# Optimization experiments

Measured on AMD Instinct MI355X. Metric: run time of the kernel, lower is better.

The kernel has to match this reference:

```python
import jax, jax.numpy as jnp
import numpy as np
import math

B, S, D = 4, 2048, 512
H, DK, DV = 8, 12, 32

def setup_inputs() -> dict:
    key = jax.random.key(0)
    ks = jax.random.split(key, 12)
    s = 0.02
    return {
        "query": jax.random.normal(ks[0], (B, S, D), jnp.float32),
        "key": jax.random.normal(ks[1], (B, S, D), jnp.float32),
        "value": jax.random.normal(ks[2], (B, S, D), jnp.float32),
        "mask": jax.random.randint(ks[3], (B, 1, S), 0, 2, jnp.int32),
        "Wq": jax.random.normal(ks[4], (D, H * DK), jnp.float32) * s,
        "bq": jnp.zeros((H * DK,), jnp.float32),
        "Wk": jax.random.normal(ks[5], (D, H * DK), jnp.float32) * s,
        "bk": jnp.zeros((H * DK,), jnp.float32),
        "Wv": jax.random.normal(ks[6], (D, H * DV), jnp.float32) * s,
        "bv": jnp.zeros((H * DV,), jnp.float32),
        "Wx": jax.random.normal(ks[7], (H * DV, D), jnp.float32) * s,
        "bx": jnp.zeros((D,), jnp.float32),
    }

def reference(query, key, value, mask, Wq, bq, Wk, bk, Wv, bv, Wx, bx):
    # mask: (B,1,S) -> (B,1,1,S) after unsqueeze(1)
    m = mask[:, None, :, :]  # (B,1,1,S)
    nb = query.shape[0]
    # projections, split heads: (B, S, H*dk) -> (B, H, S, dk)
    q = (query @ Wq + bq).reshape(nb, -1, H, DK).transpose(0, 2, 1, 3)
    k = (key @ Wk + bk).reshape(nb, -1, H, DK).transpose(0, 2, 1, 3)
    v = (value @ Wv + bv).reshape(nb, -1, H, DV).transpose(0, 2, 1, 3)
    scores = jnp.einsum("bhqd,bhkd->bhqk", q, k) / math.sqrt(DK)
    scores = jnp.where(m == 0, jnp.float32(-1e9), scores)
    p_attn = jax.nn.softmax(scores, axis=-1)
    # dropout is identity in eval mode
    x = jnp.einsum("bhqk,bhkd->bhqd", p_attn, v)  # (B,H,S,dv)
    x = x.transpose(0, 2, 1, 3).reshape(nb, -1, H * DV)
    x = x @ Wx + bx
    return (x, p_attn)
```

## Files before the change

kernel.cpp:

```cpp
#include <hip/hip_runtime.h>
#include <math.h>

#define S_LEN 2048
#define NB 4
#define NH 8

typedef short bfrag8 __attribute__((ext_vector_type(8)));
typedef float f32x16 __attribute__((ext_vector_type(16)));
typedef float f32x4 __attribute__((ext_vector_type(4)));

#if __has_builtin(__builtin_amdgcn_exp2f)
#define EXP2(x) __builtin_amdgcn_exp2f(x)
#else
#define EXP2(x) exp2f(x)
#endif

__device__ __forceinline__ unsigned short f2bf(float x) {
  union { float f; unsigned u; } v; v.f = x;
  unsigned r = v.u + 0x7FFFu + ((v.u >> 16) & 1u);
  return (unsigned short)(r >> 16);
}

__global__ __launch_bounds__(256) void transpose_w(
    const float* __restrict__ Wq, const float* __restrict__ Wk,
    const float* __restrict__ Wv, const float* __restrict__ Wx,
    unsigned short* __restrict__ wqT, unsigned short* __restrict__ wkT,
    unsigned short* __restrict__ wvT, unsigned short* __restrict__ wxT)
{
  int i = blockIdx.x * 256 + threadIdx.x;
  if (i < 49152) {
    const int n = i / 512, kk = i % 512;
    wqT[i] = f2bf(Wq[(size_t)kk * 96 + n]);
  } else if (i < 98304) {
    i -= 49152; const int n = i / 512, kk = i % 512;
    wkT[i] = f2bf(Wk[(size_t)kk * 96 + n]);
  } else if (i < 229376) {
    i -= 98304; const int n = i / 512, kk = i % 512;
    wvT[i] = f2bf(Wv[(size_t)kk * 256 + n]);
  } else if (i < 360448) {
    i -= 229376; const int n = i / 256, kk = i % 256;
    wxT[i] = f2bf(Wx[(size_t)kk * 512 + n]);
  }
}

__global__ __launch_bounds__(256) void proj_qkv(
    const float* __restrict__ query, const float* __restrict__ key_,
    const float* __restrict__ value, const int* __restrict__ mask,
    const unsigned short* __restrict__ wqT, const unsigned short* __restrict__ wkT,
    const unsigned short* __restrict__ wvT,
    const float* __restrict__ bq, const float* __restrict__ bk,
    const float* __restrict__ bv,
    unsigned short* __restrict__ q_bf, unsigned short* __restrict__ k_bf,
    unsigned short* __restrict__ vT_bf, float qscale)
{
  const int id = blockIdx.x;
  const int xcd = id & 7, j = id >> 3;
  const int bxl = j & 7, ys = j >> 3;
  const int bx = xcd * 8 + bxl;
  const int t = threadIdx.x, w = t >> 6, lane = t & 63;
  const int lo = lane & 31, hi = lane >> 5;
  const int r0 = bx * 128 + 32 * w;

  if (ys < 6) {
    const bool isq = (ys < 3);
    const float* A = isq ? query : key_;
    const unsigned short* BT = isq ? wqT : wkT;
    const float* bias = isq ? bq : bk;
    unsigned short* Cb = isq ? q_bf : k_bf;
    const float osc = isq ? qscale : 1.0f;
    const int c0 = (isq ? ys : ys - 3) * 32;

    const float* ap = A + (size_t)(r0 + lo) * 512 + hi * 8;
    const unsigned short* bp = BT + (size_t)(c0 + lo) * 512 + hi * 8;

    f32x16 acc;
#pragma unroll
    for (int r = 0; r < 16; ++r) acc[r] = 0.f;

    for (int k0 = 0; k0 < 512; k0 += 16) {
      const float4 a0 = *reinterpret_cast<const float4*>(ap + k0);
      const float4 a1 = *reinterpret_cast<const float4*>(ap + k0 + 4);
      bfrag8 af;
      af[0] = (short)f2bf(a0.x); af[1] = (short)f2bf(a0.y);
      af[2] = (short)f2bf(a0.z); af[3] = (short)f2bf(a0.w);
      af[4] = (short)f2bf(a1.x); af[5] = (short)f2bf(a1.y);
      af[6] = (short)f2bf(a1.z); af[7] = (short)f2bf(a1.w);
      const bfrag8 bf = *reinterpret_cast<const bfrag8*>(bp + k0);
      acc = __builtin_amdgcn_mfma_f32_32x32x16_bf16(af, bf, acc, 0, 0, 0);
    }

    const int c = c0 + lo;
    const int off = (c / 12) * 16 + (c % 12);
    const float bc = bias[c];
#pragma unroll
    for (int r = 0; r < 16; ++r) {
      const int grow = r0 + (r & 3) + 8 * (r >> 2) + 4 * hi;
      Cb[(size_t)grow * 128 + off] = f2bf((acc[r] + bc) * osc);
    }
    if ((c % 12) == 0) {
      const int hh = c / 12;
#pragma unroll
      for (int r = 0; r < 16; ++r) {
        const int grow = r0 + (r & 3) + 8 * (r >> 2) + 4 * hi;
        ushort4 pv;
        pv.x = isq ? (unsigned short)0x3F80
                   : ((mask[grow] != 0) ? (unsigned short)0
                                        : (unsigned short)0xCE6E);
        pv.y = 0; pv.z = 0; pv.w = 0;
        *reinterpret_cast<ushort4*>(Cb + (size_t)grow * 128 + hh * 16 + 12) = pv;
      }
    }
  } else {
    const int ct0 = (ys - 6) * 128;
    const float* ap = value + (size_t)(r0 + lo) * 512 + hi * 8;
    const unsigned short* bp = wvT + (size_t)(ct0 + lo) * 512 + hi * 8;

    f32x16 acc[4];
#pragma unroll
    for (int tt = 0; tt < 4; ++tt)
#pragma unroll
      for (int r = 0; r < 16; ++r) acc[tt][r] = 0.f;

    for (int k0 = 0; k0 < 512; k0 += 16) {
      const float4 a0 = *reinterpret_cast<const float4*>(ap + k0);
      const float4 a1 = *reinterpret_cast<const float4*>(ap + k0 + 4);
      bfrag8 af;
      af[0] = (short)f2bf(a0.x); af[1] = (short)f2bf(a0.y);
      af[2] = (short)f2bf(a0.z); af[3] = (short)f2bf(a0.w);
      af[4] = (short)f2bf(a1.x); af[5] = (short)f2bf(a1.y);
      af[6] = (short)f2bf(a1.z); af[7] = (short)f2bf(a1.w);
#pragma unroll
      for (int tt = 0; tt < 4; ++tt) {
        const bfrag8 bf = *reinterpret_cast<const bfrag8*>(
            bp + (size_t)tt * 32 * 512 + k0);
        acc[tt] = __builtin_amdgcn_mfma_f32_32x32x16_bf16(bf, af, acc[tt], 0, 0, 0);
      }
    }

    const int s = r0 + lo;
    const int bb = s >> 11, sl = s & (S_LEN - 1);
#pragma unroll
    for (int tt = 0; tt < 4; ++tt) {
#pragma unroll
      for (int r = 0; r < 16; ++r) {
        const int c = ct0 + tt * 32 + (r & 3) + 8 * (r >> 2) + 4 * hi;
        vT_bf[((size_t)(bb * 256 + c)) * S_LEN + sl] = f2bf(acc[tt][r] + bv[c]);
      }
    }
  }
}

__global__ __launch_bounds__(256) void attn_mfma(
    const unsigned short* __restrict__ q_bf,
    const unsigned short* __restrict__ k_bf,
    const unsigned short* __restrict__ vT_bf,
    float* __restrict__ p_out, unsigned short* __restrict__ x_bf)
{
  const int id = blockIdx.x + blockIdx.y * 64;
  const int xcd = id & 7, jj = id >> 3;
  const int bh = 4 * xcd + (jj >> 6);
  const int q0 = (jj & 63) * 32;
  const int b = bh >> 3, h = bh & 7;
  const int t = threadIdx.x, w = t >> 6, lane = t & 63;
  const int lo = lane & 31, hi = lane >> 5;

  __shared__ float red_lds[4][32];
  __shared__ __align__(16) char smbuf[4 * 32 * 68 * 4];
  float (*p_lds)[32][68] = reinterpret_cast<float (*)[32][68]>(smbuf);
  float (*xr)[64][20]    = reinterpret_cast<float (*)[64][20]>(smbuf);

  const bfrag8 qf = *reinterpret_cast<const bfrag8*>(
      q_bf + (size_t)(b * S_LEN + q0 + lo) * 128 + h * 16 + hi * 8);
  const unsigned short* kbase = k_bf + (size_t)b * S_LEN * 128 + h * 16 + hi * 8;

  f32x16 zc;
#pragma unroll
  for (int r = 0; r < 16; ++r) zc[r] = 0.f;

  float sum = 0.f;
  for (int ch = w * 64; ch < S_LEN; ch += 256) {
#pragma unroll
    for (int T = 0; T < 2; ++T) {
      const bfrag8 kf = *reinterpret_cast<const bfrag8*>(
          kbase + (size_t)(ch + T * 32 + lo) * 128);
      const f32x16 sc = __builtin_amdgcn_mfma_f32_32x32x16_bf16(kf, qf, zc, 0, 0, 0);
#pragma unroll
      for (int r = 0; r < 16; ++r) sum += EXP2(sc[r]);
    }
  }
  sum += __shfl_xor(sum, 32);
  if (hi == 0) red_lds[w][lo] = sum;
  __syncthreads();
  const float inv = 1.0f /
      (red_lds[0][lo] + red_lds[1][lo] + red_lds[2][lo] + red_lds[3][lo]);

  f32x16 xacc;
#pragma unroll
  for (int r = 0; r < 16; ++r) xacc[r] = 0.f;

  const unsigned short* vbase = vT_bf + (size_t)(b * 256 + h * 32 + lo) * S_LEN;
  float* pg0 = p_out + (size_t)bh * S_LEN * S_LEN + (size_t)q0 * S_LEN;

  for (int ch = w * 64; ch < S_LEN; ch += 256) {
#pragma unroll
    for (int T = 0; T < 2; ++T) {
      const bfrag8 kf = *reinterpret_cast<const bfrag8*>(
          kbase + (size_t)(ch + T * 32 + lo) * 128);
      const f32x16 sc = __builtin_amdgcn_mfma_f32_32x32x16_bf16(kf, qf, zc, 0, 0, 0);

#pragma unroll
      for (int qd = 0; qd < 4; ++qd) {
        f32x4 ev;
        ev.x = EXP2(sc[qd * 4 + 0]) * inv;
        ev.y = EXP2(sc[qd * 4 + 1]) * inv;
        ev.z = EXP2(sc[qd * 4 + 2]) * inv;
        ev.w = EXP2(sc[qd * 4 + 3]) * inv;
        *reinterpret_cast<f32x4*>(&p_lds[w][lo][T * 32 + qd * 8 + hi * 4]) = ev;
      }

#pragma unroll
      for (int m = 0; m < 2; ++m) {
        const f32x4 pa = *reinterpret_cast<const f32x4*>(
            &p_lds[w][lo][T * 32 + m * 16 + hi * 8]);
        const f32x4 pb = *reinterpret_cast<const f32x4*>(
            &p_lds[w][lo][T * 32 + m * 16 + hi * 8 + 4]);
        bfrag8 af;
        af[0] = (short)f2bf(pa.x); af[1] = (short)f2bf(pa.y);
        af[2] = (short)f2bf(pa.z); af[3] = (short)f2bf(pa.w);
        af[4] = (short)f2bf(pb.x); af[5] = (short)f2bf(pb.y);
        af[6] = (short)f2bf(pb.z); af[7] = (short)f2bf(pb.w);
        const bfrag8 vf = *reinterpret_cast<const bfrag8*>(
            vbase + ch + T * 32 + m * 16 + hi * 8);
        xacc = __builtin_amdgcn_mfma_f32_32x32x16_bf16(af, vf, xacc, 0, 0, 0);
      }
    }

    float* pg = pg0 + ch;
#pragma unroll
    for (int i = 0; i < 8; ++i) {
      const int row = i * 4 + (lane >> 4);
      const int k4  = (lane & 15) * 4;
      const f32x4 pv = *reinterpret_cast<const f32x4*>(&p_lds[w][row][k4]);
      __builtin_nontemporal_store(pv,
          reinterpret_cast<f32x4*>(pg + (size_t)row * S_LEN + k4));
    }
  }

  __syncthreads();
#pragma unroll
  for (int r = 0; r < 16; r += 4) {
    f32x4 v4; v4.x = xacc[r]; v4.y = xacc[r + 1]; v4.z = xacc[r + 2]; v4.w = xacc[r + 3];
    *reinterpret_cast<f32x4*>(&xr[w][lane][r]) = v4;
  }
  __syncthreads();
  unsigned short* xw = x_bf + (size_t)(b * S_LEN + q0) * 256 + h * 32 + lo;
#pragma unroll
  for (int j = 0; j < 4; ++j) {
    const int rr = w * 4 + j;
    const float xs = xr[0][lane][rr] + xr[1][lane][rr]
                   + xr[2][lane][rr] + xr[3][lane][rr];
    const int row = j + 8 * w + 4 * hi;
    xw[(size_t)row * 256] = f2bf(xs);
  }
}

__global__ __launch_bounds__(256) void out_proj(
    const unsigned short* __restrict__ x_bf,
    const unsigned short* __restrict__ wxT,
    const float* __restrict__ bx, float* __restrict__ out)
{
  const int id = blockIdx.x;
  const int xcd = id & 7, j = id >> 3;
  const int bxl = j & 7, by = j >> 3;
  const int bx_ = xcd * 8 + bxl;
  const int t = threadIdx.x, w = t >> 6, lane = t & 63;
  const int lo = lane & 31, hi = lane >> 5;
  const int r0 = bx_ * 128 + 32 * w;
  const int c00 = by * 128;

  const unsigned short* ap = x_bf + (size_t)(r0 + lo) * 256 + hi * 8;
  const unsigned short* bp = wxT + (size_t)(c00 + lo) * 256 + hi * 8;

  f32x16 acc[4];
#pragma unroll
  for (int tt = 0; tt < 4; ++tt)
#pragma unroll
    for (int r = 0; r < 16; ++r) acc[tt][r] = 0.f;

  for (int k0 = 0; k0 < 256; k0 += 16) {
    const bfrag8 af = *reinterpret_cast<const bfrag8*>(ap + k0);
#pragma unroll
    for (int tt = 0; tt < 4; ++tt) {
      const bfrag8 bf = *reinterpret_cast<const bfrag8*>(
          bp + (size_t)tt * 32 * 256 + k0);
      acc[tt] = __builtin_amdgcn_mfma_f32_32x32x16_bf16(af, bf, acc[tt], 0, 0, 0);
    }
  }

#pragma unroll
  for (int tt = 0; tt < 4; ++tt) {
    const int c = c00 + tt * 32 + lo;
    const float bc = bx[c];
#pragma unroll
    for (int r = 0; r < 16; ++r) {
      const int grow = r0 + (r & 3) + 8 * (r >> 2) + 4 * hi;
      out[(size_t)grow * 512 + c] = acc[tt][r] + bc;
    }
  }
}

extern "C" void kernel_launch(void* const* d_in, const int* in_sizes, int n_in,
                              void* d_out, int out_size, void* d_ws, size_t ws_size,
                              hipStream_t stream) {
  const float* query = (const float*)d_in[0];
  const float* key_  = (const float*)d_in[1];
  const float* value = (const float*)d_in[2];
  const int*   mask  = (const int*)d_in[3];
  const float* Wq = (const float*)d_in[4];
  const float* bq = (const float*)d_in[5];
  const float* Wk = (const float*)d_in[6];
  const float* bk = (const float*)d_in[7];
  const float* Wv = (const float*)d_in[8];
  const float* bv = (const float*)d_in[9];
  const float* Wx = (const float*)d_in[10];
  const float* bx = (const float*)d_in[11];

  const int M = NB * S_LEN;
  float* out_x = (float*)d_out;
  float* out_p = out_x + (size_t)M * 512;

  unsigned short* wqT  = (unsigned short*)d_ws;
  unsigned short* wkT  = wqT + 49152;
  unsigned short* wvT  = wkT + 49152;
  unsigned short* wxT  = wvT + 131072;
  unsigned short* q_bf = wxT + 131072;
  unsigned short* k_bf = q_bf + (size_t)M * 128;
  unsigned short* vT_bf = k_bf + (size_t)M * 128;
  unsigned short* x_bf = vT_bf + (size_t)NB * 256 * S_LEN;

  const float qscale = 1.4426950408889634f / sqrtf(12.0f);

  transpose_w<<<1408, 256, 0, stream>>>(Wq, Wk, Wv, Wx, wqT, wkT, wvT, wxT);

  proj_qkv<<<512, 256, 0, stream>>>(
      query, key_, value, mask, wqT, wkT, wvT, bq, bk, bv,
      q_bf, k_bf, vT_bf, qscale);

  attn_mfma<<<dim3(S_LEN / 32, NB * NH), 256, 0, stream>>>(
      q_bf, k_bf, vT_bf, out_p, x_bf);

  out_proj<<<256, 256, 0, stream>>>(x_bf, wxT, bx, out_x);
}
```

Before: 169.1 us.

## Prefetch K fragments, use packed bf16 convert, merge Q/K projection tiles

Several changes at once. The Q/K projection blocks now compute all three 32-column tiles per block, so the fp32 activations are read once instead of three times, and the grid is halved. A hardware v_cvt_pk_bf16_f32 replaces the manual rounding in fragment packing. K fragments are software-prefetched one chunk ahead in both attention passes, and the P output switches from nontemporal to ordinary stores. Risks: fewer blocks for the projection, plus different cache behaviour for the large P write.

```diff
diff --git a/kernel.cpp b/kernel.cpp
--- a/kernel.cpp
+++ b/kernel.cpp
@@ -19,6 +19,16 @@
   union { float f; unsigned u; } v; v.f = x;
   unsigned r = v.u + 0x7FFFu + ((v.u >> 16) & 1u);
   return (unsigned short)(r >> 16);
+}
+
+__device__ __forceinline__ bfrag8 pack8(float x0, float x1, float x2, float x3,
+                                        float x4, float x5, float x6, float x7) {
+  union { bfrag8 fr; unsigned u[4]; } o;
+  asm("v_cvt_pk_bf16_f32 %0, %1, %2" : "=v"(o.u[0]) : "v"(x0), "v"(x1));
+  asm("v_cvt_pk_bf16_f32 %0, %1, %2" : "=v"(o.u[1]) : "v"(x2), "v"(x3));
+  asm("v_cvt_pk_bf16_f32 %0, %1, %2" : "=v"(o.u[2]) : "v"(x4), "v"(x5));
+  asm("v_cvt_pk_bf16_f32 %0, %1, %2" : "=v"(o.u[3]) : "v"(x6), "v"(x7));
+  return o.fr;
 }
 
 __global__ __launch_bounds__(256) void transpose_w(
@@ -61,57 +71,61 @@
   const int lo = lane & 31, hi = lane >> 5;
   const int r0 = bx * 128 + 32 * w;
 
-  if (ys < 6) {
-    const bool isq = (ys < 3);
+  if (ys < 2) {
+    const bool isq = (ys == 0);
     const float* A = isq ? query : key_;
     const unsigned short* BT = isq ? wqT : wkT;
     const float* bias = isq ? bq : bk;
     unsigned short* Cb = isq ? q_bf : k_bf;
     const float osc = isq ? qscale : 1.0f;
-    const int c0 = (isq ? ys : ys - 3) * 32;
 
     const float* ap = A + (size_t)(r0 + lo) * 512 + hi * 8;
-    const unsigned short* bp = BT + (size_t)(c0 + lo) * 512 + hi * 8;
-
-    f32x16 acc;
-#pragma unroll
-    for (int r = 0; r < 16; ++r) acc[r] = 0.f;
+    const unsigned short* bp = BT + (size_t)lo * 512 + hi * 8;
+
+    f32x16 acc[3];
+#pragma unroll
+    for (int tt = 0; tt < 3; ++tt)
+#pragma unroll
+      for (int r = 0; r < 16; ++r) acc[tt][r] = 0.f;
 
     for (int k0 = 0; k0 < 512; k0 += 16) {
       const float4 a0 = *reinterpret_cast<const float4*>(ap + k0);
       const float4 a1 = *reinterpret_cast<const float4*>(ap + k0 + 4);
-      bfrag8 af;
-      af[0] = (short)f2bf(a0.x); af[1] = (short)f2bf(a0.y);
-      af[2] = (short)f2bf(a0.z); af[3] = (short)f2bf(a0.w);
-      af[4] = (short)f2bf(a1.x); af[5] = (short)f2bf(a1.y);
-      af[6] = (short)f2bf(a1.z); af[7] = (short)f2bf(a1.w);
-      const bfrag8 bf = *reinterpret_cast<const bfrag8*>(bp + k0);
-      acc = __builtin_amdgcn_mfma_f32_32x32x16_bf16(af, bf, acc, 0, 0, 0);
-    }
-
-    const int c = c0 + lo;
-    const int off = (c / 12) * 16 + (c % 12);
-    const float bc = bias[c];
-#pragma unroll
-    for (int r = 0; r < 16; ++r) {
-      const int grow = r0 + (r & 3) + 8 * (r >> 2) + 4 * hi;
-      Cb[(size_t)grow * 128 + off] = f2bf((acc[r] + bc) * osc);
-    }
-    if ((c % 12) == 0) {
-      const int hh = c / 12;
+      const bfrag8 af = pack8(a0.x, a0.y, a0.z, a0.w, a1.x, a1.y, a1.z, a1.w);
+#pragma unroll
+      for (int tt = 0; tt < 3; ++tt) {
+        const bfrag8 bf = *reinterpret_cast<const bfrag8*>(
+            bp + (size_t)tt * 32 * 512 + k0);
+        acc[tt] = __builtin_amdgcn_mfma_f32_32x32x16_bf16(af, bf, acc[tt], 0, 0, 0);
+      }
+    }
+
+#pragma unroll
+    for (int tt = 0; tt < 3; ++tt) {
+      const int c = tt * 32 + lo;
+      const int off = (c / 12) * 16 + (c % 12);
+      const float bc = bias[c];
 #pragma unroll
       for (int r = 0; r < 16; ++r) {
         const int grow = r0 + (r & 3) + 8 * (r >> 2) + 4 * hi;
-        ushort4 pv;
-        pv.x = isq ? (unsigned short)0x3F80
-                   : ((mask[grow] != 0) ? (unsigned short)0
-                                        : (unsigned short)0xCE6E);
-        pv.y = 0; pv.z = 0; pv.w = 0;
-        *reinterpret_cast<ushort4*>(Cb + (size_t)grow * 128 + hh * 16 + 12) = pv;
+        Cb[(size_t)grow * 128 + off] = f2bf((acc[tt][r] + bc) * osc);
+      }
+      if ((c % 12) == 0) {
+        const int hh = c / 12;
+#pragma unroll
+        for (int r = 0; r < 16; ++r) {
+          const int grow = r0 + (r & 3) + 8 * (r >> 2) + 4 * hi;
+          ushort4 pv;
+          pv.x = isq ? (unsigned short)0x3F80
+                     : ((mask[grow] != 0) ? (unsigned short)0
+                                          : (unsigned short)0xCE6E);
+          pv.y = 0; pv.z = 0; pv.w = 0;
+          *reinterpret_cast<ushort4*>(Cb + (size_t)grow * 128 + hh * 16 + 12) = pv;
+        }
       }
     }
   } else {
-    const int ct0 = (ys - 6) * 128;
+    const int ct0 = (ys - 2) * 128;
     const float* ap = value + (size_t)(r0 + lo) * 512 + hi * 8;
     const unsigned short* bp = wvT + (size_t)(ct0 + lo) * 512 + hi * 8;
 
@@ -124,11 +138,7 @@
     for (int k0 = 0; k0 < 512; k0 += 16) {
       const float4 a0 = *reinterpret_cast<const float4*>(ap + k0);
       const float4 a1 = *reinterpret_cast<const float4*>(ap + k0 + 4);
-      bfrag8 af;
-      af[0] = (short)f2bf(a0.x); af[1] = (short)f2bf(a0.y);
-      af[2] = (short)f2bf(a0.z); af[3] = (short)f2bf(a0.w);
-      af[4] = (short)f2bf(a1.x); af[5] = (short)f2bf(a1.y);
-      af[6] = (short)f2bf(a1.z); af[7] = (short)f2bf(a1.w);
+      const bfrag8 af = pack8(a0.x, a0.y, a0.z, a0.w, a1.x, a1.y, a1.z, a1.w);
 #pragma unroll
       for (int tt = 0; tt < 4; ++tt) {
         const bfrag8 bf = *reinterpret_cast<const bfrag8*>(
@@ -178,14 +188,22 @@
   for (int r = 0; r < 16; ++r) zc[r] = 0.f;
 
   float sum = 0.f;
-  for (int ch = w * 64; ch < S_LEN; ch += 256) {
-#pragma unroll
-    for (int T = 0; T < 2; ++T) {
-      const bfrag8 kf = *reinterpret_cast<const bfrag8*>(
-          kbase + (size_t)(ch + T * 32 + lo) * 128);
-      const f32x16 sc = __builtin_amdgcn_mfma_f32_32x32x16_bf16(kf, qf, zc, 0, 0, 0);
-#pragma unroll
-      for (int r = 0; r < 16; ++r) sum += EXP2(sc[r]);
+  {
+    bfrag8 k0 = *reinterpret_cast<const bfrag8*>(kbase + (size_t)(w * 64 + lo) * 128);
+    bfrag8 k1 = *reinterpret_cast<const bfrag8*>(kbase + (size_t)(w * 64 + 32 + lo) * 128);
+    for (int ch = w * 64; ch < S_LEN; ch += 256) {
+      const int nch = (ch + 256 < S_LEN) ? ch + 256 : ch;
+      const bfrag8 n0 = *reinterpret_cast<const bfrag8*>(
+          kbase + (size_t)(nch + lo) * 128);
+      const bfrag8 n1 = *reinterpret_cast<const bfrag8*>(
+          kbase + (size_t)(nch + 32 + lo) * 128);
+      const f32x16 s0 = __builtin_amdgcn_mfma_f32_32x32x16_bf16(k0, qf, zc, 0, 0, 0);
+#pragma unroll
+      for (int r = 0; r < 16; ++r) sum += EXP2(s0[r]);
+      const f32x16 s1 = __builtin_amdgcn_mfma_f32_32x32x16_bf16(k1, qf, zc, 0, 0, 0);
+#pragma unroll
+      for (int r = 0; r < 16; ++r) sum += EXP2(s1[r]);
+      k0 = n0; k1 = n1;
     }
   }
   sum += __shfl_xor(sum, 32);
@@ -201,12 +219,20 @@
   const unsigned short* vbase = vT_bf + (size_t)(b * 256 + h * 32 + lo) * S_LEN;
   float* pg0 = p_out + (size_t)bh * S_LEN * S_LEN + (size_t)q0 * S_LEN;
 
+  bfrag8 k0 = *reinterpret_cast<const bfrag8*>(kbase + (size_t)(w * 64 + lo) * 128);
+  bfrag8 k1 = *reinterpret_cast<const bfrag8*>(kbase + (size_t)(w * 64 + 32 + lo) * 128);
+
   for (int ch = w * 64; ch < S_LEN; ch += 256) {
+    const int nch = (ch + 256 < S_LEN) ? ch + 256 : ch;
+    const bfrag8 n0 = *reinterpret_cast<const bfrag8*>(
+        kbase + (size_t)(nch + lo) * 128);
+    const bfrag8 n1 = *reinterpret_cast<const bfrag8*>(
+        kbase + (size_t)(nch + 32 + lo) * 128);
+
 #pragma unroll
     for (int T = 0; T < 2; ++T) {
-      const bfrag8 kf = *reinterpret_cast<const bfrag8*>(
-          kbase + (size_t)(ch + T * 32 + lo) * 128);
-      const f32x16 sc = __builtin_amdgcn_mfma_f32_32x32x16_bf16(kf, qf, zc, 0, 0, 0);
+      const f32x16 sc = __builtin_amdgcn_mfma_f32_32x32x16_bf16(
+          T ? k1 : k0, qf, zc, 0, 0, 0);
 
 #pragma unroll
       for (int qd = 0; qd < 4; ++qd) {
@@ -224,11 +250,7 @@
             &p_lds[w][lo][T * 32 + m * 16 + hi * 8]);
         const f32x4 pb = *reinterpret_cast<const f32x4*>(
             &p_lds[w][lo][T * 32 + m * 16 + hi * 8 + 4]);
-        bfrag8 af;
-        af[0] = (short)f2bf(pa.x); af[1] = (short)f2bf(pa.y);
-        af[2] = (short)f2bf(pa.z); af[3] = (short)f2bf(pa.w);
-        af[4] = (short)f2bf(pb.x); af[5] = (short)f2bf(pb.y);
-        af[6] = (short)f2bf(pb.z); af[7] = (short)f2bf(pb.w);
+        const bfrag8 af = pack8(pa.x, pa.y, pa.z, pa.w, pb.x, pb.y, pb.z, pb.w);
         const bfrag8 vf = *reinterpret_cast<const bfrag8*>(
             vbase + ch + T * 32 + m * 16 + hi * 8);
         xacc = __builtin_amdgcn_mfma_f32_32x32x16_bf16(af, vf, xacc, 0, 0, 0);
@@ -241,9 +263,9 @@
       const int row = i * 4 + (lane >> 4);
       const int k4  = (lane & 15) * 4;
       const f32x4 pv = *reinterpret_cast<const f32x4*>(&p_lds[w][row][k4]);
-      __builtin_nontemporal_store(pv,
-          reinterpret_cast<f32x4*>(pg + (size_t)row * S_LEN + k4));
-    }
+      *reinterpret_cast<f32x4*>(pg + (size_t)row * S_LEN + k4) = pv;
+    }
+    k0 = n0; k1 = n1;
   }
 
   __syncthreads();
@@ -342,7 +364,7 @@
 
   transpose_w<<<1408, 256, 0, stream>>>(Wq, Wk, Wv, Wx, wqT, wkT, wvT, wxT);
 
-  proj_qkv<<<512, 256, 0, stream>>>(
+  proj_qkv<<<256, 256, 0, stream>>>(
       query, key_, value, mask, wqT, wkT, wvT, bq, bk, bv,
       q_bf, k_bf, vT_bf, qscale);
 
```

New measurement: 183.3 us. 8.4% more time.
